# Performance work log

Measured on AMD Instinct MI355X. Metric: run time of the kernel, lower is better.

The kernel has to match this reference:

```python
import jax, jax.numpy as jnp
import numpy as np
import math

E, H, T, B = 1024, 16, 2048, 2
HD = E // H  # 64
NUM_BUCKETS, MAX_DIST = 32, 128


def setup_inputs() -> dict:
    key = jax.random.key(0)
    ks = jax.random.split(key, 8)
    s = 0.02
    return {
        'query': jax.random.normal(ks[0], (T, B, E), jnp.float32),
        'q_w': jax.random.normal(ks[1], (E, E), jnp.float32) * s,
        'q_b': jnp.zeros((E,), jnp.float32),
        'k_w': jax.random.normal(ks[2], (E, E), jnp.float32) * s,
        'k_b': jnp.zeros((E,), jnp.float32),
        'v_w': jax.random.normal(ks[3], (E, E), jnp.float32) * s,
        'v_b': jnp.zeros((E,), jnp.float32),
        'out_w': jax.random.normal(ks[4], (E, E), jnp.float32) * s,
        'out_b': jnp.zeros((E,), jnp.float32),
        'rel_emb': jax.random.normal(ks[5], (NUM_BUCKETS, H), jnp.float32) * s,
        'grep_w': jax.random.normal(ks[6], (8, HD), jnp.float32) * s,
        'grep_b': jnp.zeros((8,), jnp.float32),
        'grep_a': jnp.ones((1, H, 1, 1), jnp.float32),
    }


def _rel_bucket(rp):
    # bidirectional T5-style bucketing, num_buckets=32 -> nb=16, max_exact=8
    nb = NUM_BUCKETS // 2
    buckets = (rp > 0).astype(jnp.int32) * nb
    rpa = jnp.abs(rp)
    max_exact = nb // 2
    large = max_exact + (
        jnp.log(jnp.maximum(rpa, 1).astype(jnp.float32) / max_exact)
        / math.log(MAX_DIST / max_exact) * (nb - max_exact)
    ).astype(jnp.int32)
    large = jnp.minimum(large, nb - 1)
    return buckets + jnp.where(rpa < max_exact, rpa, large)


def reference(query, q_w, q_b, k_w, k_b, v_w, v_b, out_w, out_b, rel_emb, grep_w, grep_b, grep_a):
    t, b, e = query.shape
    scaling = HD ** -0.5
    # relative-position bucket bias -> [H, T, T]
    rp = jnp.arange(t)[None, :] - jnp.arange(t)[:, None]  # memory - context
    pos_bias = jnp.transpose(rel_emb[_rel_bucket(rp)], (2, 0, 1))  # [H,T,T]
    # GRU-style gate computed from the RAW query (pre q_proj)
    ql = jnp.transpose(query, (1, 0, 2)).reshape(b, t, H, HD).transpose(0, 2, 1, 3)  # [B,H,T,HD]
    gate_in = (ql @ grep_w.T + grep_b).reshape(b, H, t, 2, 4).sum(-1)  # [B,H,T,2]
    gate = jax.nn.sigmoid(gate_in)
    gate_a, gate_b = gate[..., 0:1], gate[..., 1:2]  # each [B,H,T,1]
    gate_a_1 = gate_a * (gate_b * grep_a - 1.0) + 2.0  # [B,H,T,1]
    bias = gate_a_1 * pos_bias[None]  # [B,H,T,T]
    # projections (self-attention: key = value = query)
    q = (query @ q_w.T + q_b) * scaling
    k = query @ k_w.T + k_b
    v = query @ v_w.T + v_b
    qh = q.reshape(t, b, H, HD)
    kh = k.reshape(t, b, H, HD)
    vh = v.reshape(t, b, H, HD)
    scores = jnp.einsum('tbhd,sbhd->bhts', qh, kh) + bias
    attn = jax.nn.softmax(scores, axis=-1)
    out = jnp.einsum('bhts,sbhd->tbhd', attn, vh).reshape(t, b, e)
    return out @ out_w.T + out_b
```

## Files before the change

kernel.cpp:

```cpp
#include <hip/hip_runtime.h>
#include <math.h>

typedef unsigned short u16;
typedef unsigned int u32;
typedef __bf16 bf16x8 __attribute__((ext_vector_type(8)));
typedef float f32x4 __attribute__((ext_vector_type(4)));
typedef float f32x16 __attribute__((ext_vector_type(16)));

__device__ __forceinline__ u32 f2bf(float f) {
  union { float f; u32 u; } v; v.f = f;
  u32 r = v.u + 0x7fffu + ((v.u >> 16) & 1u);
  return r >> 16;
}

__device__ __forceinline__ u32 pkbf(float a, float b) {
  u32 r;
  asm("v_cvt_pk_bf16_f32 %0, %1, %2" : "=v"(r) : "v"(a), "v"(b));
  return r;
}

__device__ __forceinline__ float ex2(float x) {
  float r;
  asm("v_exp_f32 %0, %1" : "=v"(r) : "v"(x));
  return r;
}

__device__ __forceinline__ void gld16(const void* g, void* s) {
  __builtin_amdgcn_global_load_lds(
      reinterpret_cast<__attribute__((address_space(1))) u32*>((size_t)g),
      reinterpret_cast<__attribute__((address_space(3))) u32*>((u32)(size_t)s),
      16, 0, 0);
}

__global__ __launch_bounds__(256) void prepk(
    const float* __restrict__ query, const float* __restrict__ q_w,
    const float* __restrict__ k_w, const float* __restrict__ v_w,
    const float* __restrict__ out_w, const float* __restrict__ rel_emb,
    const float* __restrict__ grep_w, const float* __restrict__ grep_b,
    const float* __restrict__ grep_a,
    u16* __restrict__ qbf, u16* __restrict__ wqb, u16* __restrict__ wkb,
    u16* __restrict__ wvb, u16* __restrict__ wob,
    float* __restrict__ lut, float* __restrict__ gate) {
  const int bid = blockIdx.x, tid = threadIdx.x;
  if (bid < 8192) {
    const float* src; u16* dst; int i0;
    if (bid < 4096)      { src = query; dst = qbf; i0 = bid; }
    else if (bid < 5120) { src = q_w;   dst = wqb; i0 = bid - 4096; }
    else if (bid < 6144) { src = k_w;   dst = wkb; i0 = bid - 5120; }
    else if (bid < 7168) { src = v_w;   dst = wvb; i0 = bid - 6144; }
    else                 { src = out_w; dst = wob; i0 = bid - 7168; }
    const int i = i0 * 256 + tid;
    float4 v = ((const float4*)src)[i];
    uint2 o;
    o.x = f2bf(v.x) | (f2bf(v.y) << 16);
    o.y = f2bf(v.z) | (f2bf(v.w) << 16);
    ((uint2*)dst)[i] = o;
  } else if (bid < 8208) {
    const int dix = (bid - 8192) * 256 + tid;
    int rp = dix - 2048;
    int bucket = (rp > 0) ? 16 : 0;
    int rpa = rp < 0 ? -rp : rp;
    if (rpa < 8) {
      bucket += rpa;
    } else {
      int large = 8 + (int)(logf((float)rpa * 0.125f) * (8.0f / 2.772588722239781f));
      bucket += (large < 15) ? large : 15;
    }
    const float LOG2E = 1.4426950408889634f;
#pragma unroll
    for (int h = 0; h < 16; ++h) lut[h * 4096 + dix] = rel_emb[bucket * 16 + h] * LOG2E;
  } else {
    __shared__ __align__(16) float gw[8][64];
    __shared__ float gb[8];
    __shared__ float ga[16];
    if (tid < 128) ((float4*)&gw[0][0])[tid] = ((const float4*)grep_w)[tid];
    if (tid < 8) gb[tid] = grep_b[tid];
    if (tid < 16) ga[tid] = grep_a[tid];
    __syncthreads();
    const int i = (bid - 8208) * 256 + tid;
    const int t = i & 2047, h = (i >> 11) & 15, b = i >> 15;
    const float* x = query + ((size_t)t * 2 + b) * 1024 + h * 64;
    float acc[8] = {0, 0, 0, 0, 0, 0, 0, 0};
    for (int e4 = 0; e4 < 16; ++e4) {
      float4 xv = ((const float4*)x)[e4];
#pragma unroll
      for (int j = 0; j < 8; ++j)
        acc[j] += xv.x * gw[j][e4 * 4] + xv.y * gw[j][e4 * 4 + 1] +
                  xv.z * gw[j][e4 * 4 + 2] + xv.w * gw[j][e4 * 4 + 3];
    }
    float sA = acc[0] + acc[1] + acc[2] + acc[3] + gb[0] + gb[1] + gb[2] + gb[3];
    float sB = acc[4] + acc[5] + acc[6] + acc[7] + gb[4] + gb[5] + gb[6] + gb[7];
    float gA = 1.0f / (1.0f + expf(-sA));
    float gB = 1.0f / (1.0f + expf(-sB));
    gate[i] = gA * (gB * ga[h] - 1.0f) + 2.0f;
  }
}

template <int MB, int NM>
__global__ __launch_bounds__(256) void gemmk(
    const u16* __restrict__ A,
    const u16* __restrict__ W0, const u16* __restrict__ W1, const u16* __restrict__ W2,
    const float* __restrict__ b0, const float* __restrict__ b1, const float* __restrict__ b2,
    u16* __restrict__ qa, u16* __restrict__ kst, u16* __restrict__ vst,
    float* __restrict__ fout) {
  __shared__ __align__(16) u16 As[64 * 64];
  __shared__ __align__(16) u16 Bs[NM][64 * 64];

  const int tid = threadIdx.x;
  const int l = tid & 63;
  const int w = tid >> 6;
  const int wr = w >> 1, wc = w & 1;
  const int m0 = blockIdx.y * 64, n0 = blockIdx.x * 64;
  const int li = l >> 3, ls = l & 7;
  const u16* const Ws[3] = {W0, W1, W2};
  const float* const bs[3] = {b0, b1, b2};

  f32x4 acc[NM][2][2] = {};

  for (int k0 = 0; k0 < 1024; k0 += 64) {
#pragma unroll
    for (int j = 0; j < 2; ++j) {
      const int rr = w * 16 + j * 8 + li;
      const int cs = ls ^ (rr & 7);
      gld16(A + ((size_t)(m0 + rr) << 10) + k0 + cs * 8, &As[(w * 16 + j * 8) * 64]);
#pragma unroll
      for (int mm = 0; mm < NM; ++mm)
        gld16(Ws[mm] + ((size_t)(n0 + rr) << 10) + k0 + cs * 8, &Bs[mm][(w * 16 + j * 8) * 64]);
    }
    __syncthreads();
#pragma unroll
    for (int ks = 0; ks < 2; ++ks) {
      bf16x8 af[2];
#pragma unroll
      for (int mf = 0; mf < 2; ++mf) {
        const int row = wr * 32 + mf * 16 + (l & 15);
        const int slot = (ks * 4 + (l >> 4)) ^ (row & 7);
        af[mf] = *(const bf16x8*)&As[row * 64 + slot * 8];
      }
#pragma unroll
      for (int mm = 0; mm < NM; ++mm) {
        bf16x8 bfr[2];
#pragma unroll
        for (int nf = 0; nf < 2; ++nf) {
          const int row = wc * 32 + nf * 16 + (l & 15);
          const int slot = (ks * 4 + (l >> 4)) ^ (row & 7);
          bfr[nf] = *(const bf16x8*)&Bs[mm][row * 64 + slot * 8];
        }
#pragma unroll
        for (int mf = 0; mf < 2; ++mf)
#pragma unroll
          for (int nf = 0; nf < 2; ++nf)
            acc[mm][mf][nf] = __builtin_amdgcn_mfma_f32_16x16x32_bf16(af[mf], bfr[nf], acc[mm][mf][nf], 0, 0, 0);
      }
    }
    __syncthreads();
  }

  const float QSC = 0.125f * 1.4426950408889634f;
#pragma unroll
  for (int mm = 0; mm < NM; ++mm) {
    const int mode = MB + mm;
    const float* bias = bs[mm];
#pragma unroll
    for (int mf = 0; mf < 2; ++mf)
#pragma unroll
      for (int nf = 0; nf < 2; ++nf)
#pragma unroll
        for (int r = 0; r < 4; ++r) {
          const int row = m0 + wr * 32 + mf * 16 + (l >> 4) * 4 + r;
          const int col = n0 + wc * 32 + nf * 16 + (l & 15);
          float v = acc[mm][mf][nf][r] + bias[col];
          const int t = row >> 1, bb = row & 1, hh = col >> 6, d = col & 63;
          const size_t bh = (size_t)bb * 16 + hh;
          if (mode == 0) {
            v *= QSC;
            qa[((bh * 2048 + t) << 6) + d] = (u16)f2bf(v);
          } else if (mode == 1) {
            kst[((bh * 64 + (t >> 5)) << 11) + ((d >> 3) << 8) + ((t & 31) << 3) + (d & 7)] = (u16)f2bf(v);
          } else if (mode == 2) {
            vst[((bh * 64 + (t >> 5)) << 11) + (((t >> 3) & 3) << 9) + (d << 3) + (t & 7)] = (u16)f2bf(v);
          } else {
            fout[((size_t)row << 10) + col] = v;
          }
        }
  }
}

__global__ __launch_bounds__(256, 4) void flashk(const u16* __restrict__ qa,
                                                 const u16* __restrict__ kst,
                                                 const u16* __restrict__ vst,
                                                 const float* __restrict__ lutg,
                                                 const float* __restrict__ gatew,
                                                 u16* __restrict__ aout) {
  const int B = blockIdx.x;
  const int xcd = B & 7, j = B >> 3;
  const int bh = xcd * 4 + (j >> 5);
  const int qt = j & 31;
  const int hh = bh & 15, b = bh >> 4;
  const int tid = threadIdx.x, l = tid & 63, w = tid >> 6;
  const int half = w >> 1, sub = w & 1;
  const int hi = l >> 5, q = l & 31;
  const int q0b = qt * 64;
  const int q0w = q0b + sub * 32;
  const int qg = q0w + q;

  __shared__ union {
    struct { u16 K[2][2][2048]; u16 V[2][2][2048]; } m;
    struct { float pm[4][32]; float pl[4][32]; float pO[4][32][68]; } c;
  } S;
  __shared__ __align__(16) float slice[288];

  for (int i = tid; i < 288; i += 256) slice[i] = lutg[hh * 4096 + 1920 + i];

  const size_t tb0 = (size_t)bh * 64;
  const u16* Q = qa + ((size_t)bh << 17);

  bf16x8 qf[4];
#pragma unroll
  for (int mk = 0; mk < 4; ++mk)
    qf[mk] = *(const bf16x8*)&Q[((size_t)qg << 6) + mk * 16 + hi * 8];

  const float g = gatew[((size_t)bh << 11) + qg];
  const float gcm = g * lutg[hh * 4096];
  const float gcp = g * lutg[hh * 4096 + 4095];

  float m_run = -3e38f, l_run = 0.0f;
  f32x16 oacc[2] = {};

  {
    const u16* kt0 = kst + ((tb0 + half * 32) << 11) + l * 8;
    const u16* vt0 = vst + ((tb0 + half * 32) << 11) + l * 8;
    if (sub == 0) {
#pragma unroll
      for (int i = 0; i < 4; ++i) gld16(kt0 + i * 512, &S.m.K[half][0][i * 512]);
    } else {
#pragma unroll
      for (int i = 0; i < 4; ++i) gld16(vt0 + i * 512, &S.m.V[half][0][i * 512]);
    }
  }
  __syncthreads();

  for (int ts = 0; ts < 32; ++ts) {
    const int bf_ = ts & 1;
    if (ts < 31) {
      const u16* ktn = kst + ((tb0 + half * 32 + ts + 1) << 11) + l * 8;
      const u16* vtn = vst + ((tb0 + half * 32 + ts + 1) << 11) + l * 8;
      if (sub == 0) {
#pragma unroll
        for (int i = 0; i < 4; ++i) gld16(ktn + i * 512, &S.m.K[half][bf_ ^ 1][i * 512]);
      } else {
#pragma unroll
        for (int i = 0; i < 4; ++i) gld16(vtn + i * 512, &S.m.V[half][bf_ ^ 1][i * 512]);
      }
    }
    const u16* Kb = &S.m.K[half][bf_][0];
    const u16* Vb = &S.m.V[half][bf_][0];
    const int s0 = half * 1024 + ts * 32;

    f32x16 s = {};
#pragma unroll
    for (int mk = 0; mk < 4; ++mk) {
      bf16x8 kf = *(const bf16x8*)&Kb[(mk * 2 + hi) * 256 + q * 8];
      s = __builtin_amdgcn_mfma_f32_32x32x16_bf16(kf, qf[mk], s, 0, 0, 0);
    }

    const int kt = (s0 - q0w) >> 5;
    const bool far = (kt <= -4) | (kt >= 4);
    float gc = 0.0f;
    float mx;
    if (far) {
      gc = (kt < 0) ? gcm : gcp;
      float t0_ = fmaxf(fmaxf(s[0], s[1]), s[2]);
      float t1_ = fmaxf(fmaxf(s[3], s[4]), s[5]);
      float t2_ = fmaxf(fmaxf(s[6], s[7]), s[8]);
      float t3_ = fmaxf(fmaxf(s[9], s[10]), s[11]);
      float t4_ = fmaxf(fmaxf(s[12], s[13]), s[14]);
      mx = fmaxf(fmaxf(fmaxf(t0_, t1_), t2_), fmaxf(fmaxf(t3_, t4_), s[15]));
      mx = fmaxf(mx, __shfl_xor(mx, 32, 64)) + gc;
    } else {
      const int sb = s0 - q0w + 128 + 4 * hi - q;
#pragma unroll
      for (int reg = 0; reg < 16; ++reg) {
        const int kloc = (reg & 3) + 8 * (reg >> 2);
        s[reg] = fmaf(g, slice[sb + kloc], s[reg]);
      }
      float t0_ = fmaxf(fmaxf(s[0], s[1]), s[2]);
      float t1_ = fmaxf(fmaxf(s[3], s[4]), s[5]);
      float t2_ = fmaxf(fmaxf(s[6], s[7]), s[8]);
      float t3_ = fmaxf(fmaxf(s[9], s[10]), s[11]);
      float t4_ = fmaxf(fmaxf(s[12], s[13]), s[14]);
      mx = fmaxf(fmaxf(fmaxf(t0_, t1_), t2_), fmaxf(fmaxf(t3_, t4_), s[15]));
      mx = fmaxf(mx, __shfl_xor(mx, 32, 64));
    }
    if (!__all(mx - m_run <= 11.5f)) {
      const float mnew = fmaxf(m_run, mx);
      const float sc = ex2(m_run - mnew);
      l_run *= sc;
#pragma unroll
      for (int r = 0; r < 16; ++r) { oacc[0][r] *= sc; oacc[1][r] *= sc; }
      m_run = mnew;
    }
    const float mref = m_run - gc;
#pragma unroll
    for (int reg = 0; reg < 16; ++reg) s[reg] = ex2(s[reg] - mref);
    {
      float r0 = (s[0] + s[1]) + (s[2] + s[3]);
      float r1 = (s[4] + s[5]) + (s[6] + s[7]);
      float r2 = (s[8] + s[9]) + (s[10] + s[11]);
      float r3 = (s[12] + s[13]) + (s[14] + s[15]);
      float rsum = (r0 + r1) + (r2 + r3);
      rsum += __shfl_xor(rsum, 32, 64);
      l_run += rsum;
    }
    bf16x8 pa[2];
#pragma unroll
    for (int kh = 0; kh < 2; ++kh) {
      const int rb = kh * 8;
      const u32 X0 = pkbf(s[rb + 0], s[rb + 1]);
      const u32 X1 = pkbf(s[rb + 2], s[rb + 3]);
      const u32 Y0 = pkbf(s[rb + 4], s[rb + 5]);
      const u32 Y1 = pkbf(s[rb + 6], s[rb + 7]);
      const u32 E0 = hi ? X0 : Y0;
      const u32 E1 = hi ? X1 : Y1;
      const u32 Ep0 = (u32)__shfl_xor((int)E0, 32, 64);
      const u32 Ep1 = (u32)__shfl_xor((int)E1, 32, 64);
      union { u32 wds[4]; bf16x8 v; } pu;
      pu.wds[0] = hi ? Ep0 : X0;
      pu.wds[1] = hi ? Ep1 : X1;
      pu.wds[2] = hi ? Y0 : Ep0;
      pu.wds[3] = hi ? Y1 : Ep1;
      pa[kh] = pu.v;
    }
#pragma unroll
    for (int dt = 0; dt < 2; ++dt)
#pragma unroll
      for (int kh = 0; kh < 2; ++kh) {
        bf16x8 vf = *(const bf16x8*)&Vb[(kh * 2 + hi) * 512 + dt * 256 + q * 8];
        oacc[dt] = __builtin_amdgcn_mfma_f32_32x32x16_bf16(vf, pa[kh], oacc[dt], 0, 0, 0);
      }
    __syncthreads();
  }

  __syncthreads();
  if (hi == 0) { S.c.pm[w][q] = m_run; S.c.pl[w][q] = l_run; }
#pragma unroll
  for (int dt = 0; dt < 2; ++dt)
#pragma unroll
    for (int g4 = 0; g4 < 4; ++g4) {
      float4 v4;
      v4.x = oacc[dt][g4 * 4 + 0];
      v4.y = oacc[dt][g4 * 4 + 1];
      v4.z = oacc[dt][g4 * 4 + 2];
      v4.w = oacc[dt][g4 * 4 + 3];
      *(float4*)&S.c.pO[w][q][dt * 32 + g4 * 8 + hi * 4] = v4;
    }
  __syncthreads();

  const int rr = tid >> 2;
  const int dc = (tid & 3) << 4;
  const int rl = rr & 31, sr = rr >> 5;
  const float mA = S.c.pm[sr][rl], mB = S.c.pm[2 + sr][rl];
  const float M = fmaxf(mA, mB);
  const float eA = ex2(mA - M), eB = ex2(mB - M);
  const float inv = 1.0f / (S.c.pl[sr][rl] * eA + S.c.pl[2 + sr][rl] * eB);
  union { u16 hb[16]; uint4 u4[2]; } st;
#pragma unroll
  for (int c4 = 0; c4 < 4; ++c4) {
    const float4 a = *(const float4*)&S.c.pO[sr][rl][dc + c4 * 4];
    const float4 bb = *(const float4*)&S.c.pO[2 + sr][rl][dc + c4 * 4];
    st.hb[c4 * 4 + 0] = (u16)f2bf((a.x * eA + bb.x * eB) * inv);
    st.hb[c4 * 4 + 1] = (u16)f2bf((a.y * eA + bb.y * eB) * inv);
    st.hb[c4 * 4 + 2] = (u16)f2bf((a.z * eA + bb.z * eB) * inv);
    st.hb[c4 * 4 + 3] = (u16)f2bf((a.w * eA + bb.w * eB) * inv);
  }
  u16* dst = &aout[(((size_t)(q0b + rr) * 2 + b) << 10) + hh * 64 + dc];
  *(uint4*)dst = st.u4[0];
  *(uint4*)(dst + 8) = st.u4[1];
}

extern "C" void kernel_launch(void* const* d_in, const int* in_sizes, int n_in,
                              void* d_out, int out_size, void* d_ws, size_t ws_size,
                              hipStream_t stream) {
  (void)in_sizes; (void)n_in; (void)out_size; (void)ws_size;
  const float* query  = (const float*)d_in[0];
  const float* q_w    = (const float*)d_in[1];
  const float* q_b    = (const float*)d_in[2];
  const float* k_w    = (const float*)d_in[3];
  const float* k_b    = (const float*)d_in[4];
  const float* v_w    = (const float*)d_in[5];
  const float* v_b    = (const float*)d_in[6];
  const float* out_w  = (const float*)d_in[7];
  const float* out_b  = (const float*)d_in[8];
  const float* rel_emb= (const float*)d_in[9];
  const float* grep_w = (const float*)d_in[10];
  const float* grep_b = (const float*)d_in[11];
  const float* grep_a = (const float*)d_in[12];

  char* ws = (char*)d_ws;
  const size_t MB = 1ull << 20;
  u16* qbf  = (u16*)(ws + 0 * MB);
  u16* wqb  = (u16*)(ws + 8 * MB);
  u16* wkb  = (u16*)(ws + 10 * MB);
  u16* wvb  = (u16*)(ws + 12 * MB);
  u16* wob  = (u16*)(ws + 14 * MB);
  u16* qav  = (u16*)(ws + 16 * MB);
  u16* kstg = (u16*)(ws + 24 * MB);
  u16* vstg = (u16*)(ws + 32 * MB);
  u16* aout = (u16*)(ws + 40 * MB);
  float* lut  = (float*)(ws + 48 * MB);
  float* gate = (float*)(ws + 48 * MB + 256 * 1024);

  prepk<<<dim3(8464), 256, 0, stream>>>(query, q_w, k_w, v_w, out_w, rel_emb,
                                        grep_w, grep_b, grep_a,
                                        qbf, wqb, wkb, wvb, wob, lut, gate);

  gemmk<0, 3><<<dim3(16, 64), 256, 0, stream>>>(qbf, wqb, wkb, wvb, q_b, k_b, v_b,
                                                qav, kstg, vstg, nullptr);
  flashk<<<dim3(1024), 256, 0, stream>>>(qav, kstg, vstg, lut, gate, aout);
  gemmk<3, 1><<<dim3(16, 64), 256, 0, stream>>>(aout, wob, wob, wob, out_b, out_b, out_b,
                                                nullptr, nullptr, nullptr, (float*)d_out);
}
```

Measured before the change: 143.1 us.

## Process two query tiles per wave in flash kernel to reuse K/V fragments

```diff
diff --git a/kernel.cpp b/kernel.cpp
--- a/kernel.cpp
+++ b/kernel.cpp
@@ -186,7 +186,7 @@
   }
 }
 
-__global__ __launch_bounds__(256, 4) void flashk(const u16* __restrict__ qa,
+__global__ __launch_bounds__(256, 2) void flashk(const u16* __restrict__ qa,
                                                  const u16* __restrict__ kst,
                                                  const u16* __restrict__ vst,
                                                  const float* __restrict__ lutg,
@@ -194,20 +194,21 @@
                                                  u16* __restrict__ aout) {
   const int B = blockIdx.x;
   const int xcd = B & 7, j = B >> 3;
-  const int bh = xcd * 4 + (j >> 5);
-  const int qt = j & 31;
+  const int bh = xcd * 4 + (j >> 4);
+  const int qt = j & 15;
   const int hh = bh & 15, b = bh >> 4;
   const int tid = threadIdx.x, l = tid & 63, w = tid >> 6;
   const int half = w >> 1, sub = w & 1;
   const int hi = l >> 5, q = l & 31;
-  const int q0b = qt * 64;
-  const int q0w = q0b + sub * 32;
-  const int qg = q0w + q;
+  const int q0b = qt * 128;
+  const int qr0 = q0b + sub * 32;
+  const int qr1 = q0b + 64 + sub * 32;
 
   __shared__ union {
     struct { u16 K[2][2][2048]; u16 V[2][2][2048]; } m;
-    struct { float pm[4][32]; float pl[4][32]; float pO[4][32][68]; } c;
+    struct { float pO[2][2][32][68]; } c;
   } S;
+  __shared__ float pm[2][2][32], pl[2][2][32];
   __shared__ __align__(16) float slice[288];
 
   for (int i = tid; i < 288; i += 256) slice[i] = lutg[hh * 4096 + 1920 + i];
@@ -215,17 +216,21 @@
   const size_t tb0 = (size_t)bh * 64;
   const u16* Q = qa + ((size_t)bh << 17);
 
-  bf16x8 qf[4];
-#pragma unroll
-  for (int mk = 0; mk < 4; ++mk)
-    qf[mk] = *(const bf16x8*)&Q[((size_t)qg << 6) + mk * 16 + hi * 8];
-
-  const float g = gatew[((size_t)bh << 11) + qg];
-  const float gcm = g * lutg[hh * 4096];
-  const float gcp = g * lutg[hh * 4096 + 4095];
-
-  float m_run = -3e38f, l_run = 0.0f;
-  f32x16 oacc[2] = {};
+  bf16x8 qf[2][4];
+  float g[2], m_run[2], l_run[2];
+  f32x16 oacc[2][2] = {};
+#pragma unroll
+  for (int qi = 0; qi < 2; ++qi) {
+    const int qg = (qi ? qr1 : qr0) + q;
+#pragma unroll
+    for (int mk = 0; mk < 4; ++mk)
+      qf[qi][mk] = *(const bf16x8*)&Q[((size_t)qg << 6) + mk * 16 + hi * 8];
+    g[qi] = gatew[((size_t)bh << 11) + qg];
+    m_run[qi] = -3e38f;
+    l_run[qi] = 0.0f;
+  }
+  const float lutm = lutg[hh * 4096];
+  const float lutp = lutg[hh * 4096 + 4095];
 
   {
     const u16* kt0 = kst + ((tb0 + half * 32) << 11) + l * 8;
@@ -257,125 +262,149 @@
     const u16* Vb = &S.m.V[half][bf_][0];
     const int s0 = half * 1024 + ts * 32;
 
-    f32x16 s = {};
-#pragma unroll
-    for (int mk = 0; mk < 4; ++mk) {
-      bf16x8 kf = *(const bf16x8*)&Kb[(mk * 2 + hi) * 256 + q * 8];
-      s = __builtin_amdgcn_mfma_f32_32x32x16_bf16(kf, qf[mk], s, 0, 0, 0);
-    }
-
-    const int kt = (s0 - q0w) >> 5;
-    const bool far = (kt <= -4) | (kt >= 4);
-    float gc = 0.0f;
-    float mx;
-    if (far) {
-      gc = (kt < 0) ? gcm : gcp;
-      float t0_ = fmaxf(fmaxf(s[0], s[1]), s[2]);
-      float t1_ = fmaxf(fmaxf(s[3], s[4]), s[5]);
-      float t2_ = fmaxf(fmaxf(s[6], s[7]), s[8]);
-      float t3_ = fmaxf(fmaxf(s[9], s[10]), s[11]);
-      float t4_ = fmaxf(fmaxf(s[12], s[13]), s[14]);
-      mx = fmaxf(fmaxf(fmaxf(t0_, t1_), t2_), fmaxf(fmaxf(t3_, t4_), s[15]));
-      mx = fmaxf(mx, __shfl_xor(mx, 32, 64)) + gc;
-    } else {
-      const int sb = s0 - q0w + 128 + 4 * hi - q;
-#pragma unroll
-      for (int reg = 0; reg < 16; ++reg) {
-        const int kloc = (reg & 3) + 8 * (reg >> 2);
-        s[reg] = fmaf(g, slice[sb + kloc], s[reg]);
-      }
-      float t0_ = fmaxf(fmaxf(s[0], s[1]), s[2]);
-      float t1_ = fmaxf(fmaxf(s[3], s[4]), s[5]);
-      float t2_ = fmaxf(fmaxf(s[6], s[7]), s[8]);
-      float t3_ = fmaxf(fmaxf(s[9], s[10]), s[11]);
-      float t4_ = fmaxf(fmaxf(s[12], s[13]), s[14]);
-      mx = fmaxf(fmaxf(fmaxf(t0_, t1_), t2_), fmaxf(fmaxf(t3_, t4_), s[15]));
-      mx = fmaxf(mx, __shfl_xor(mx, 32, 64));
-    }
-    if (!__all(mx - m_run <= 11.5f)) {
-      const float mnew = fmaxf(m_run, mx);
-      const float sc = ex2(m_run - mnew);
-      l_run *= sc;
-#pragma unroll
-      for (int r = 0; r < 16; ++r) { oacc[0][r] *= sc; oacc[1][r] *= sc; }
-      m_run = mnew;
-    }
-    const float mref = m_run - gc;
-#pragma unroll
-    for (int reg = 0; reg < 16; ++reg) s[reg] = ex2(s[reg] - mref);
-    {
-      float r0 = (s[0] + s[1]) + (s[2] + s[3]);
-      float r1 = (s[4] + s[5]) + (s[6] + s[7]);
-      float r2 = (s[8] + s[9]) + (s[10] + s[11]);
-      float r3 = (s[12] + s[13]) + (s[14] + s[15]);
-      float rsum = (r0 + r1) + (r2 + r3);
-      rsum += __shfl_xor(rsum, 32, 64);
-      l_run += rsum;
-    }
-    bf16x8 pa[2];
-#pragma unroll
-    for (int kh = 0; kh < 2; ++kh) {
-      const int rb = kh * 8;
-      const u32 X0 = pkbf(s[rb + 0], s[rb + 1]);
-      const u32 X1 = pkbf(s[rb + 2], s[rb + 3]);
-      const u32 Y0 = pkbf(s[rb + 4], s[rb + 5]);
-      const u32 Y1 = pkbf(s[rb + 6], s[rb + 7]);
-      const u32 E0 = hi ? X0 : Y0;
-      const u32 E1 = hi ? X1 : Y1;
-      const u32 Ep0 = (u32)__shfl_xor((int)E0, 32, 64);
-      const u32 Ep1 = (u32)__shfl_xor((int)E1, 32, 64);
-      union { u32 wds[4]; bf16x8 v; } pu;
-      pu.wds[0] = hi ? Ep0 : X0;
-      pu.wds[1] = hi ? Ep1 : X1;
-      pu.wds[2] = hi ? Y0 : Ep0;
-      pu.wds[3] = hi ? Y1 : Ep1;
-      pa[kh] = pu.v;
-    }
-#pragma unroll
-    for (int dt = 0; dt < 2; ++dt)
+    bf16x8 kf[4];
+#pragma unroll
+    for (int mk = 0; mk < 4; ++mk)
+      kf[mk] = *(const bf16x8*)&Kb[(mk * 2 + hi) * 256 + q * 8];
+
+    bf16x8 pa[2][2];
+#pragma unroll
+    for (int qi = 0; qi < 2; ++qi) {
+      const int qrb = qi ? qr1 : qr0;
+      f32x16 s = {};
+#pragma unroll
+      for (int mk = 0; mk < 4; ++mk)
+        s = __builtin_amdgcn_mfma_f32_32x32x16_bf16(kf[mk], qf[qi][mk], s, 0, 0, 0);
+
+      const int kt = (s0 - qrb) >> 5;
+      const bool far = (kt <= -4) | (kt >= 4);
+      float gc = 0.0f;
+      float mx;
+      if (far) {
+        gc = ((kt < 0) ? lutm : lutp) * g[qi];
+        float t0_ = fmaxf(fmaxf(s[0], s[1]), s[2]);
+        float t1_ = fmaxf(fmaxf(s[3], s[4]), s[5]);
+        float t2_ = fmaxf(fmaxf(s[6], s[7]), s[8]);
+        float t3_ = fmaxf(fmaxf(s[9], s[10]), s[11]);
+        float t4_ = fmaxf(fmaxf(s[12], s[13]), s[14]);
+        mx = fmaxf(fmaxf(fmaxf(t0_, t1_), t2_), fmaxf(fmaxf(t3_, t4_), s[15]));
+        mx = fmaxf(mx, __shfl_xor(mx, 32, 64)) + gc;
+      } else {
+        const int sb = s0 - qrb + 128 + 4 * hi - q;
+#pragma unroll
+        for (int reg = 0; reg < 16; ++reg) {
+          const int kloc = (reg & 3) + 8 * (reg >> 2);
+          s[reg] = fmaf(g[qi], slice[sb + kloc], s[reg]);
+        }
+        float t0_ = fmaxf(fmaxf(s[0], s[1]), s[2]);
+        float t1_ = fmaxf(fmaxf(s[3], s[4]), s[5]);
+        float t2_ = fmaxf(fmaxf(s[6], s[7]), s[8]);
+        float t3_ = fmaxf(fmaxf(s[9], s[10]), s[11]);
+        float t4_ = fmaxf(fmaxf(s[12], s[13]), s[14]);
+        mx = fmaxf(fmaxf(fmaxf(t0_, t1_), t2_), fmaxf(fmaxf(t3_, t4_), s[15]));
+        mx = fmaxf(mx, __shfl_xor(mx, 32, 64));
+      }
+      if (!__all(mx - m_run[qi] <= 11.5f)) {
+        const float mnew = fmaxf(m_run[qi], mx);
+        const float sc = ex2(m_run[qi] - mnew);
+        l_run[qi] *= sc;
+#pragma unroll
+        for (int r = 0; r < 16; ++r) { oacc[qi][0][r] *= sc; oacc[qi][1][r] *= sc; }
+        m_run[qi] = mnew;
+      }
+      const float mref = m_run[qi] - gc;
+#pragma unroll
+      for (int reg = 0; reg < 16; ++reg) s[reg] = ex2(s[reg] - mref);
+      {
+        float r0 = (s[0] + s[1]) + (s[2] + s[3]);
+        float r1 = (s[4] + s[5]) + (s[6] + s[7]);
+        float r2 = (s[8] + s[9]) + (s[10] + s[11]);
+        float r3 = (s[12] + s[13]) + (s[14] + s[15]);
+        float rsum = (r0 + r1) + (r2 + r3);
+        rsum += __shfl_xor(rsum, 32, 64);
+        l_run[qi] += rsum;
+      }
 #pragma unroll
       for (int kh = 0; kh < 2; ++kh) {
-        bf16x8 vf = *(const bf16x8*)&Vb[(kh * 2 + hi) * 512 + dt * 256 + q * 8];
-        oacc[dt] = __builtin_amdgcn_mfma_f32_32x32x16_bf16(vf, pa[kh], oacc[dt], 0, 0, 0);
-      }
+        const int rb = kh * 8;
+        const u32 X0 = pkbf(s[rb + 0], s[rb + 1]);
+        const u32 X1 = pkbf(s[rb + 2], s[rb + 3]);
+        const u32 Y0 = pkbf(s[rb + 4], s[rb + 5]);
+        const u32 Y1 = pkbf(s[rb + 6], s[rb + 7]);
+        const u32 E0 = hi ? X0 : Y0;
+        const u32 E1 = hi ? X1 : Y1;
+        const u32 Ep0 = (u32)__shfl_xor((int)E0, 32, 64);
+        const u32 Ep1 = (u32)__shfl_xor((int)E1, 32, 64);
+        union { u32 wds[4]; bf16x8 v; } pu;
+        pu.wds[0] = hi ? Ep0 : X0;
+        pu.wds[1] = hi ? Ep1 : X1;
+        pu.wds[2] = hi ? Y0 : Ep0;
+        pu.wds[3] = hi ? Y1 : Ep1;
+        pa[qi][kh] = pu.v;
+      }
+    }
+    bf16x8 vf[4];
+#pragma unroll
+    for (int i2 = 0; i2 < 4; ++i2) {
+      const int dt = i2 >> 1, kh = i2 & 1;
+      vf[i2] = *(const bf16x8*)&Vb[(kh * 2 + hi) * 512 + dt * 256 + q * 8];
+    }
+#pragma unroll
+    for (int qi = 0; qi < 2; ++qi)
+#pragma unroll
+      for (int dt = 0; dt < 2; ++dt)
+#pragma unroll
+        for (int kh = 0; kh < 2; ++kh)
+          oacc[qi][dt] = __builtin_amdgcn_mfma_f32_32x32x16_bf16(vf[dt * 2 + kh], pa[qi][kh], oacc[qi][dt], 0, 0, 0);
     __syncthreads();
   }
 
   __syncthreads();
-  if (hi == 0) { S.c.pm[w][q] = m_run; S.c.pl[w][q] = l_run; }
-#pragma unroll
-  for (int dt = 0; dt < 2; ++dt)
-#pragma unroll
-    for (int g4 = 0; g4 < 4; ++g4) {
-      float4 v4;
-      v4.x = oacc[dt][g4 * 4 + 0];
-      v4.y = oacc[dt][g4 * 4 + 1];
-      v4.z = oacc[dt][g4 * 4 + 2];
-      v4.w = oacc[dt][g4 * 4 + 3];
-      *(float4*)&S.c.pO[w][q][dt * 32 + g4 * 8 + hi * 4] = v4;
-    }
+  if (half == 1) {
+    if (hi == 0) {
+      pm[sub][0][q] = m_run[0]; pl[sub][0][q] = l_run[0];
+      pm[sub][1][q] = m_run[1]; pl[sub][1][q] = l_run[1];
+    }
+#pragma unroll
+    for (int qi = 0; qi < 2; ++qi)
+#pragma unroll
+      for (int dt = 0; dt < 2; ++dt)
+#pragma unroll
+        for (int g4 = 0; g4 < 4; ++g4) {
+          float4 v4;
+          v4.x = oacc[qi][dt][g4 * 4 + 0];
+          v4.y = oacc[qi][dt][g4 * 4 + 1];
+          v4.z = oacc[qi][dt][g4 * 4 + 2];
+          v4.w = oacc[qi][dt][g4 * 4 + 3];
+          *(float4*)&S.c.pO[sub][qi][q][dt * 32 + g4 * 8 + hi * 4] = v4;
+        }
+  }
   __syncthreads();
-
-  const int rr = tid >> 2;
-  const int dc = (tid & 3) << 4;
-  const int rl = rr & 31, sr = rr >> 5;
-  const float mA = S.c.pm[sr][rl], mB = S.c.pm[2 + sr][rl];
-  const float M = fmaxf(mA, mB);
-  const float eA = ex2(mA - M), eB = ex2(mB - M);
-  const float inv = 1.0f / (S.c.pl[sr][rl] * eA + S.c.pl[2 + sr][rl] * eB);
-  union { u16 hb[16]; uint4 u4[2]; } st;
-#pragma unroll
-  for (int c4 = 0; c4 < 4; ++c4) {
-    const float4 a = *(const float4*)&S.c.pO[sr][rl][dc + c4 * 4];
-    const float4 bb = *(const float4*)&S.c.pO[2 + sr][rl][dc + c4 * 4];
-    st.hb[c4 * 4 + 0] = (u16)f2bf((a.x * eA + bb.x * eB) * inv);
-    st.hb[c4 * 4 + 1] = (u16)f2bf((a.y * eA + bb.y * eB) * inv);
-    st.hb[c4 * 4 + 2] = (u16)f2bf((a.z * eA + bb.z * eB) * inv);
-    st.hb[c4 * 4 + 3] = (u16)f2bf((a.w * eA + bb.w * eB) * inv);
-  }
-  u16* dst = &aout[(((size_t)(q0b + rr) * 2 + b) << 10) + hh * 64 + dc];
-  *(uint4*)dst = st.u4[0];
-  *(uint4*)(dst + 8) = st.u4[1];
+  if (half == 0) {
+#pragma unroll
+    for (int qi = 0; qi < 2; ++qi) {
+      const float mB = pm[sub][qi][q], lB = pl[sub][qi][q];
+      const float M = fmaxf(m_run[qi], mB);
+      const float eA = ex2(m_run[qi] - M), eB = ex2(mB - M);
+      const float inv = 1.0f / (l_run[qi] * eA + lB * eB);
+      const int qg = (qi ? qr1 : qr0) + q;
+#pragma unroll
+      for (int dt = 0; dt < 2; ++dt)
+#pragma unroll
+        for (int gph = 0; gph < 4; ++gph) {
+          const int d0 = dt * 32 + gph * 8 + hi * 4;
+          const float4 p4 = *(const float4*)&S.c.pO[sub][qi][q][d0];
+          const float o0 = (oacc[qi][dt][gph * 4 + 0] * eA + p4.x * eB) * inv;
+          const float o1 = (oacc[qi][dt][gph * 4 + 1] * eA + p4.y * eB) * inv;
+          const float o2 = (oacc[qi][dt][gph * 4 + 2] * eA + p4.z * eB) * inv;
+          const float o3 = (oacc[qi][dt][gph * 4 + 3] * eA + p4.w * eB) * inv;
+          uint2 st;
+          st.x = pkbf(o0, o1);
+          st.y = pkbf(o2, o3);
+          *(uint2*)&aout[(((size_t)qg * 2 + b) << 10) + hh * 64 + d0] = st;
+        }
+    }
+  }
 }
 
 extern "C" void kernel_launch(void* const* d_in, const int* in_sizes, int n_in,
@@ -416,7 +445,7 @@
 
   gemmk<0, 3><<<dim3(16, 64), 256, 0, stream>>>(qbf, wqb, wkb, wvb, q_b, k_b, v_b,
                                                 qav, kstg, vstg, nullptr);
-  flashk<<<dim3(1024), 256, 0, stream>>>(qav, kstg, vstg, lut, gate, aout);
+  flashk<<<dim3(512), 256, 0, stream>>>(qav, kstg, vstg, lut, gate, aout);
   gemmk<3, 1><<<dim3(16, 64), 256, 0, stream>>>(aout, wob, wob, wob, out_b, out_b, out_b,
                                                 nullptr, nullptr, nullptr, (float*)d_out);
 }
```

After: 138.2 us (median of 2 runs). 1.04x faster.
